# Performance work log

Measured on AMD Instinct MI355X. Metric: run time of the kernel, lower is better.

The kernel has to match this reference:

```python
import jax, jax.numpy as jnp
import numpy as np

N_NODES = 50000  # 4 node types x 12500
N_PER = 12500
E = 600000
H = 128
IN_DIMS = [128, 128, 64, 64]


def setup_inputs() -> dict:
    key = jax.random.key(0)
    ks = jax.random.split(key, 16)
    inp = {}
    for i, d in enumerate(IN_DIMS):
        inp[f"feat{i}"] = jax.random.normal(ks[i], (N_PER, d), dtype=jnp.float32)
        # xavier_normal-ish init, gain 1.414
        std = 1.414 * np.sqrt(2.0 / (d + H))
        inp[f"W_fc{i}"] = jax.random.normal(ks[4 + i], (d, H), dtype=jnp.float32) * std
        inp[f"b_fc{i}"] = jnp.zeros((H,), dtype=jnp.float32)
    inp["src"] = jax.random.randint(ks[8], (E,), 0, N_NODES, dtype=jnp.int32)
    inp["dst"] = jax.random.randint(ks[9], (E,), 0, N_NODES, dtype=jnp.int32)
    inp["e_feat"] = jax.random.randint(ks[10], (E,), 0, 36, dtype=jnp.int32)
    inp["b_g0"] = jnp.zeros((H,), dtype=jnp.float32)  # GraphConv layer0 (weight=False, bias)
    inp["W_g1"] = jax.random.normal(ks[11], (H, H), dtype=jnp.float32) * np.sqrt(1.0 / H)
    inp["b_g1"] = jnp.zeros((H,), dtype=jnp.float32)
    return inp


def _degree_norms(src, dst):
    ones = jnp.ones((src.shape[0],), dtype=jnp.float32)
    deg_out = jax.ops.segment_sum(ones, src, num_segments=N_NODES)
    deg_in = jax.ops.segment_sum(ones, dst, num_segments=N_NODES)
    # DGL norm='both': D_out^{-1/2} on src side, D_in^{-1/2} on dst side (clamp 0-degree)
    out_norm = jax.lax.rsqrt(jnp.maximum(deg_out, 1.0))
    in_norm = jax.lax.rsqrt(jnp.maximum(deg_in, 1.0))
    return out_norm, in_norm


def _gcn_aggregate(h, src, dst, out_norm, in_norm):
    m = (h * out_norm[:, None])[src]                      # [E, H] gather
    agg = jax.ops.segment_sum(m, dst, num_segments=N_NODES)
    return agg * in_norm[:, None]


def reference(feat0, feat1, feat2, feat3,
              W_fc0, b_fc0, W_fc1, b_fc1, W_fc2, b_fc2, W_fc3, b_fc3,
              src, dst, e_feat, b_g0, W_g1, b_g1):
    # per-node-type linear projections, then concat along node dim
    h = jnp.concatenate([
        feat0 @ W_fc0 + b_fc0,
        feat1 @ W_fc1 + b_fc1,
        feat2 @ W_fc2 + b_fc2,
        feat3 @ W_fc3 + b_fc3,
    ], axis=0)  # [N_NODES, H]

    out_norm, in_norm = _degree_norms(src, dst)
    # GraphConv layer 0: weight=False, bias, activation (dropout p=0 -> identity)
    h = jax.nn.relu(_gcn_aggregate(h, src, dst, out_norm, in_norm) + b_g0)
    # GraphConv layer 1: aggregate, then linear weight + bias, activation
    h = jax.nn.relu(_gcn_aggregate(h, src, dst, out_norm, in_norm) @ W_g1 + b_g1)

    e = e_feat.astype(jnp.float32)  # e_feat.reshape(-1,1).float() in original
    # forward graph: msg = ft + sum_{r in 0..4} where(e==r, ft, 0) = ft * (1 + 1{e in 0..4})
    w_fwd = 1.0 + sum((e == float(r)).astype(jnp.float32) for r in (0, 1, 2, 3, 4))
    agg_a = jax.ops.segment_sum(h[src] * w_fwd[:, None], dst, num_segments=N_NODES)
    # transpose graph (reversed edges, same e): msg = sum_{r in {6,14,30}} where(e==r, ft, 0)
    w_bwd = sum((e == float(r)).astype(jnp.float32) for r in (6, 14, 30))
    agg_b = jax.ops.segment_sum(h[dst] * w_bwd[:, None], src, num_segments=N_NODES)
    return agg_a + agg_b
```

## Files before the change

### kernel.cpp

```cpp
#include <hip/hip_runtime.h>
#include <hip/hip_bf16.h>

#define N_NODES 50000
#define N_PER   12500
#define E_EDGES 600000
#define HDIM    128

#define NBLK_BUILD ((E_EDGES + 255) / 256)
#define NBLK_FC    ((N_PER + 63) / 64)
#define BK_CAP  32
#define BKB_CAP 8
#define MASK31  0x7fffffff

#define HQ 32
#define HP 4
#define HSLICE (E_EDGES / HQ)

typedef __attribute__((ext_vector_type(8))) short bfrag;
typedef __attribute__((ext_vector_type(4))) float ffrag;

__device__ __forceinline__ unsigned short f2bf(float f) {
    union { float f; unsigned u; } x; x.f = f;
    unsigned r = x.u + 0x7fffu + ((x.u >> 16) & 1u);
    return (unsigned short)(r >> 16);
}
__device__ __forceinline__ float lo_bf(unsigned v) { return __uint_as_float(v << 16); }
__device__ __forceinline__ float hi_bf(unsigned v) { return __uint_as_float(v & 0xffff0000u); }
__device__ __forceinline__ unsigned pack2(float a, float b) {
    return (unsigned)f2bf(a) | ((unsigned)f2bf(b) << 16);
}
__device__ __forceinline__ float onrm_of(int deg) {
    return rsqrtf(fmaxf((float)deg, 1.0f));
}

__device__ __forceinline__ void acc8_add(float* acc, uint4 v) {
    acc[0] += lo_bf(v.x); acc[1] += hi_bf(v.x);
    acc[2] += lo_bf(v.y); acc[3] += hi_bf(v.y);
    acc[4] += lo_bf(v.z); acc[5] += hi_bf(v.z);
    acc[6] += lo_bf(v.w); acc[7] += hi_bf(v.w);
}
__device__ __forceinline__ void acc8_addw(float* acc, uint4 v, float w) {
    acc[0] += lo_bf(v.x) * w; acc[1] += hi_bf(v.x) * w;
    acc[2] += lo_bf(v.y) * w; acc[3] += hi_bf(v.y) * w;
    acc[4] += lo_bf(v.z) * w; acc[5] += hi_bf(v.z) * w;
    acc[6] += lo_bf(v.w) * w; acc[7] += hi_bf(v.w) * w;
}

__global__ __launch_bounds__(256) void prep_kernel(
    const float* __restrict__ W0, const float* __restrict__ W1,
    const float* __restrict__ W2, const float* __restrict__ W3,
    const float* __restrict__ Wg,
    const int* __restrict__ src,
    unsigned short* __restrict__ Wp, int* __restrict__ initp,
    unsigned short* __restrict__ partial) {
    __shared__ int hist[N_PER];
    int b = blockIdx.x;
    if (b < HQ * HP) {
        const int q = b >> 2;
        const int p = b & 3;
        for (int j = threadIdx.x; j < N_PER; j += 256) hist[j] = 0;
        __syncthreads();
        const int e0 = q * HSLICE;
        for (int i = e0 + threadIdx.x; i < e0 + HSLICE; i += 256) {
            int s = src[i];
            unsigned r = (unsigned)(s - p * N_PER);
            if (r < (unsigned)N_PER) atomicAdd(&hist[r], 1);
        }
        __syncthreads();
        unsigned short* out = partial + (size_t)q * N_NODES + (size_t)p * N_PER;
        for (int j = threadIdx.x; j < N_PER; j += 256)
            out[j] = (unsigned short)hist[j];
    } else if (b < HQ * HP + 32) {
        int tid = (b - HQ * HP) * 256 + threadIdx.x;
        const float* W; int D, base, off;
        if      (tid < 2048) { W = W0; D = 128; base = 0;    off = 0;     }
        else if (tid < 4096) { W = W1; D = 128; base = 2048; off = 16384; }
        else if (tid < 5120) { W = W2; D = 64;  base = 4096; off = 32768; }
        else if (tid < 6144) { W = W3; D = 64;  base = 5120; off = 40960; }
        else                 { W = Wg; D = 128; base = 6144; off = 49152; }
        int t2 = tid - base;
        int KT = D / 32;
        int l = t2 & 63;
        int tt = t2 >> 6;
        int kt = tt % KT, n0 = tt / KT;
        int n = n0 * 16 + (l & 15);
        int kb = kt * 32 + (l >> 4) * 8;
#pragma unroll
        for (int j = 0; j < 8; ++j)
            Wp[(size_t)off + (size_t)t2 * 8 + j] = f2bf(W[(size_t)(kb + j) * 128 + n]);
    } else {
        int blk = b - (HQ * HP + 32);
#pragma unroll
        for (int k = 0; k < 4; ++k) {
            int i = blk * 1024 + k * 256 + threadIdx.x;
            if (i < 4 * N_NODES)
                initp[i] = (i < 2 * N_NODES) ? -1 : 0;
        }
    }
}

template<int D>
__device__ __forceinline__ void fc_body(
    int blk, int tid,
    const float* __restrict__ X,
    const unsigned short* __restrict__ Wp,
    const float* __restrict__ bias,
    unsigned short* __restrict__ outbf,
    int rows)
{
    constexpr int KT = D / 32;
    const int lane = tid & 63;
    const int wave = tid >> 6;
    const int m = lane & 15, q = lane >> 4;
    const int rbase = blk * 64 + wave * 16;
    const int row = rbase + m;

    bfrag afr[KT];
#pragma unroll
    for (int kt = 0; kt < KT; ++kt) {
        bfrag a;
        if (row < rows) {
            const float* xp = X + (size_t)row * D + kt * 32 + q * 8;
            float4 u0 = *(const float4*)xp;
            float4 u1 = *(const float4*)(xp + 4);
            a[0] = (short)f2bf(u0.x); a[1] = (short)f2bf(u0.y);
            a[2] = (short)f2bf(u0.z); a[3] = (short)f2bf(u0.w);
            a[4] = (short)f2bf(u1.x); a[5] = (short)f2bf(u1.y);
            a[6] = (short)f2bf(u1.z); a[7] = (short)f2bf(u1.w);
        } else {
#pragma unroll
            for (int t = 0; t < 8; ++t) a[t] = 0;
        }
        afr[kt] = a;
    }

    ffrag acc[8];
#pragma unroll
    for (int n0 = 0; n0 < 8; ++n0)
#pragma unroll
        for (int t = 0; t < 4; ++t) acc[n0][t] = 0.f;

#pragma unroll
    for (int n0 = 0; n0 < 8; ++n0)
#pragma unroll
        for (int kt = 0; kt < KT; ++kt) {
            bfrag bfr = *(const bfrag*)(Wp + ((size_t)(n0 * KT + kt) * 64 + lane) * 8);
            acc[n0] = __builtin_amdgcn_mfma_f32_16x16x32_bf16(afr[kt], bfr, acc[n0], 0, 0, 0);
        }

#pragma unroll
    for (int n0 = 0; n0 < 8; ++n0) {
        const int col = n0 * 16 + m;
        const float bj = bias[col];
#pragma unroll
        for (int r = 0; r < 4; ++r) {
            int orow = rbase + q * 4 + r;
            if (orow < rows)
                outbf[(size_t)orow * 128 + col] = f2bf(acc[n0][r] + bj);
        }
    }
}

__global__ __launch_bounds__(256) void mega_kernel(
    const int* __restrict__ src, const int* __restrict__ dst,
    const int* __restrict__ ef,
    int* __restrict__ cnt_in, int* __restrict__ cntB,
    int* __restrict__ bucket, int* __restrict__ bucketB,
    int* __restrict__ head_ov, int* __restrict__ ov_pay, int* __restrict__ ov_nxt,
    int* __restrict__ head_ovB, int* __restrict__ ovB_pay, int* __restrict__ ovB_nxt,
    const float* __restrict__ f0, const float* __restrict__ f1,
    const float* __restrict__ f2, const float* __restrict__ f3,
    const unsigned short* __restrict__ Wp,
    const float* __restrict__ b0, const float* __restrict__ b1,
    const float* __restrict__ b2, const float* __restrict__ b3,
    unsigned short* __restrict__ Abf)
{
    const int b = blockIdx.x;
    if (b < NBLK_BUILD) {
        int e = b * 256 + threadIdx.x;
        if (e >= E_EDGES) return;
        int s = src[e], d = dst[e], t = ef[e];
        int v = s | ((t <= 4) ? 0x80000000 : 0);
        int p = atomicAdd(&cnt_in[d], 1);
        if (p < BK_CAP) bucket[d * BK_CAP + p] = v;
        else { ov_pay[e] = v; ov_nxt[e] = atomicExch(&head_ov[d], e); }
        if (t == 6 || t == 14 || t == 30) {
            int p2 = atomicAdd(&cntB[s], 1);
            if (p2 < BKB_CAP) bucketB[s * BKB_CAP + p2] = d;
            else { ovB_pay[e] = d; ovB_nxt[e] = atomicExch(&head_ovB[s], e); }
        }
    } else {
        int fb = b - NBLK_BUILD;
        int which = fb / NBLK_FC;
        int blk = fb - which * NBLK_FC;
        if (which == 0)
            fc_body<128>(blk, threadIdx.x, f0, Wp,         b0, Abf + (size_t)0 * N_PER * HDIM, N_PER);
        else if (which == 1)
            fc_body<128>(blk, threadIdx.x, f1, Wp + 16384, b1, Abf + (size_t)1 * N_PER * HDIM, N_PER);
        else if (which == 2)
            fc_body<64>(blk, threadIdx.x, f2, Wp + 32768, b2, Abf + (size_t)2 * N_PER * HDIM, N_PER);
        else
            fc_body<64>(blk, threadIdx.x, f3, Wp + 40960, b3, Abf + (size_t)3 * N_PER * HDIM, N_PER);
    }
}

__global__ __launch_bounds__(256) void scale_kernel(
    uint4* __restrict__ A, const unsigned short* __restrict__ partial,
    float* __restrict__ onrm_buf) {
    int idx = blockIdx.x * blockDim.x + threadIdx.x;
    int n = idx >> 4, j8 = idx & 15;
    int d = (int)partial[(size_t)j8 * N_NODES + n]
          + (int)partial[(size_t)(j8 + 16) * N_NODES + n];
    d += __shfl_xor(d, 1);
    d += __shfl_xor(d, 2);
    d += __shfl_xor(d, 4);
    d += __shfl_xor(d, 8);
    float on = onrm_of(d);
    if (j8 == 0) onrm_buf[n] = on;
    uint4 v = A[(size_t)n * 16 + j8];
    uint4 o;
    o.x = pack2(lo_bf(v.x) * on, hi_bf(v.x) * on);
    o.y = pack2(lo_bf(v.y) * on, hi_bf(v.y) * on);
    o.z = pack2(lo_bf(v.z) * on, hi_bf(v.z) * on);
    o.w = pack2(lo_bf(v.w) * on, hi_bf(v.w) * on);
    A[(size_t)n * 16 + j8] = o;
}

__global__ __launch_bounds__(256) void agg0_kernel(
    const uint4* __restrict__ A,
    const int* __restrict__ bucket, const int* __restrict__ cnt_in,
    const int* __restrict__ head_ov, const int* __restrict__ ov_pay,
    const int* __restrict__ ov_nxt,
    const float* __restrict__ onrm_buf, const float* __restrict__ b_g0,
    uint4* __restrict__ B) {
    int idx = blockIdx.x * blockDim.x + threadIdx.x;
    int n = idx >> 4, j8 = idx & 15;
    const int cnt = cnt_in[n];
    const int* bk = bucket + (size_t)n * BK_CAP;
    float acc[8] = {0.f, 0.f, 0.f, 0.f, 0.f, 0.f, 0.f, 0.f};
    int lim = min(cnt, BK_CAP);
    int i = 0;
    for (; i + 4 <= lim; i += 4) {
        int s0 = bk[i] & MASK31,     s1 = bk[i + 1] & MASK31;
        int s2 = bk[i + 2] & MASK31, s3 = bk[i + 3] & MASK31;
        uint4 v0 = A[(size_t)s0 * 16 + j8];
        uint4 v1 = A[(size_t)s1 * 16 + j8];
        uint4 v2 = A[(size_t)s2 * 16 + j8];
        uint4 v3 = A[(size_t)s3 * 16 + j8];
        acc8_add(acc, v0); acc8_add(acc, v1);
        acc8_add(acc, v2); acc8_add(acc, v3);
    }
    for (; i < lim; ++i) {
        int s = bk[i] & MASK31;
        acc8_add(acc, A[(size_t)s * 16 + j8]);
    }
    if (cnt > BK_CAP) {
        int e = head_ov[n];
        while (e >= 0) {
            int s = ov_pay[e] & MASK31;
            acc8_add(acc, A[(size_t)s * 16 + j8]);
            e = ov_nxt[e];
        }
    }
    float inr = onrm_of(cnt);
    float onr = onrm_buf[n];
    const float* bg = b_g0 + j8 * 8;
    float r[8];
#pragma unroll
    for (int k = 0; k < 8; ++k)
        r[k] = fmaxf(acc[k] * inr + bg[k], 0.f) * onr;
    uint4 o;
    o.x = pack2(r[0], r[1]); o.y = pack2(r[2], r[3]);
    o.z = pack2(r[4], r[5]); o.w = pack2(r[6], r[7]);
    B[(size_t)n * 16 + j8] = o;
}

__global__ __launch_bounds__(256) void gemm1_fused_kernel(
    const unsigned short* __restrict__ Bbf,
    const int* __restrict__ bucket, const int* __restrict__ cnt_in,
    const int* __restrict__ head_ov, const int* __restrict__ ov_pay,
    const int* __restrict__ ov_nxt,
    const unsigned short* __restrict__ Wp, const float* __restrict__ bias,
    unsigned short* __restrict__ outbf)
{
    const int lane = threadIdx.x & 63;
    const int wave = threadIdx.x >> 6;
    const int m = lane & 15, q = lane >> 4;
    const int rbase = blockIdx.x * 64 + wave * 16;
    const int node = rbase + m;

    float ga[32];
#pragma unroll
    for (int i = 0; i < 32; ++i) ga[i] = 0.f;

    if (node < N_NODES) {
        const int cnt = cnt_in[node];
        const int* bk = bucket + (size_t)node * BK_CAP;
        int lim = min(cnt, BK_CAP);
        int i = 0;
        for (; i + 2 <= lim; i += 2) {
            int s0 = bk[i] & MASK31, s1 = bk[i + 1] & MASK31;
            const uint4* r0 = (const uint4*)(Bbf + (size_t)s0 * 128);
            const uint4* r1 = (const uint4*)(Bbf + (size_t)s1 * 128);
            uint4 a0 = r0[0 * 4 + q], a1 = r0[1 * 4 + q], a2 = r0[2 * 4 + q], a3 = r0[3 * 4 + q];
            uint4 c0 = r1[0 * 4 + q], c1 = r1[1 * 4 + q], c2 = r1[2 * 4 + q], c3 = r1[3 * 4 + q];
            acc8_add(ga +  0, a0); acc8_add(ga +  8, a1);
            acc8_add(ga + 16, a2); acc8_add(ga + 24, a3);
            acc8_add(ga +  0, c0); acc8_add(ga +  8, c1);
            acc8_add(ga + 16, c2); acc8_add(ga + 24, c3);
        }
        for (; i < lim; ++i) {
            int s = bk[i] & MASK31;
            const uint4* rp = (const uint4*)(Bbf + (size_t)s * 128);
#pragma unroll
            for (int kt = 0; kt < 4; ++kt) acc8_add(ga + kt * 8, rp[kt * 4 + q]);
        }
        if (cnt > BK_CAP) {
            int e = head_ov[node];
            while (e >= 0) {
                int s = ov_pay[e] & MASK31;
                const uint4* rp = (const uint4*)(Bbf + (size_t)s * 128);
#pragma unroll
                for (int kt = 0; kt < 4; ++kt) acc8_add(ga + kt * 8, rp[kt * 4 + q]);
                e = ov_nxt[e];
            }
        }
    }

    bfrag afr[4];
#pragma unroll
    for (int kt = 0; kt < 4; ++kt)
#pragma unroll
        for (int j = 0; j < 8; ++j)
            afr[kt][j] = (short)f2bf(ga[kt * 8 + j]);

    ffrag acc[8];
#pragma unroll
    for (int n0 = 0; n0 < 8; ++n0)
#pragma unroll
        for (int t = 0; t < 4; ++t) acc[n0][t] = 0.f;

#pragma unroll
    for (int n0 = 0; n0 < 8; ++n0)
#pragma unroll
        for (int kt = 0; kt < 4; ++kt) {
            bfrag bfr = *(const bfrag*)(Wp + ((size_t)(n0 * 4 + kt) * 64 + lane) * 8);
            acc[n0] = __builtin_amdgcn_mfma_f32_16x16x32_bf16(afr[kt], bfr, acc[n0], 0, 0, 0);
        }

    float ir[4];
#pragma unroll
    for (int r = 0; r < 4; ++r) {
        int orow = rbase + q * 4 + r;
        ir[r] = (orow < N_NODES) ? onrm_of(cnt_in[orow]) : 0.f;
    }
#pragma unroll
    for (int n0 = 0; n0 < 8; ++n0) {
        const int col = n0 * 16 + m;
        const float bj = bias[col];
#pragma unroll
        for (int r = 0; r < 4; ++r) {
            int orow = rbase + q * 4 + r;
            if (orow < N_NODES)
                outbf[(size_t)orow * 128 + col] = f2bf(fmaxf(acc[n0][r] * ir[r] + bj, 0.f));
        }
    }
}

__global__ __launch_bounds__(256) void final_kernel(
    const uint4* __restrict__ H,
    const int* __restrict__ bucket, const int* __restrict__ cnt_in,
    const int* __restrict__ head_ov, const int* __restrict__ ov_pay,
    const int* __restrict__ ov_nxt,
    const int* __restrict__ bucketB, const int* __restrict__ cntB,
    const int* __restrict__ head_ovB, const int* __restrict__ ovB_pay,
    const int* __restrict__ ovB_nxt,
    float4* __restrict__ out4) {
    int idx = blockIdx.x * blockDim.x + threadIdx.x;
    int n = idx >> 4, j8 = idx & 15;
    float acc[8] = {0.f, 0.f, 0.f, 0.f, 0.f, 0.f, 0.f, 0.f};
    const int cnt = cnt_in[n];
    const int* bk = bucket + (size_t)n * BK_CAP;
    int lim = min(cnt, BK_CAP);
    int i = 0;
    for (; i + 4 <= lim; i += 4) {
        int c0 = bk[i], c1 = bk[i + 1], c2 = bk[i + 2], c3 = bk[i + 3];
        uint4 v0 = H[(size_t)(c0 & MASK31) * 16 + j8];
        uint4 v1 = H[(size_t)(c1 & MASK31) * 16 + j8];
        uint4 v2 = H[(size_t)(c2 & MASK31) * 16 + j8];
        uint4 v3 = H[(size_t)(c3 & MASK31) * 16 + j8];
        acc8_addw(acc, v0, (c0 < 0) ? 2.0f : 1.0f);
        acc8_addw(acc, v1, (c1 < 0) ? 2.0f : 1.0f);
        acc8_addw(acc, v2, (c2 < 0) ? 2.0f : 1.0f);
        acc8_addw(acc, v3, (c3 < 0) ? 2.0f : 1.0f);
    }
    for (; i < lim; ++i) {
        int c = bk[i];
        acc8_addw(acc, H[(size_t)(c & MASK31) * 16 + j8], (c < 0) ? 2.0f : 1.0f);
    }
    if (cnt > BK_CAP) {
        int e = head_ov[n];
        while (e >= 0) {
            int c = ov_pay[e];
            acc8_addw(acc, H[(size_t)(c & MASK31) * 16 + j8], (c < 0) ? 2.0f : 1.0f);
            e = ov_nxt[e];
        }
    }
    const int cb = cntB[n];
    const int* bkB = bucketB + (size_t)n * BKB_CAP;
    int limB = min(cb, BKB_CAP);
    for (int k = 0; k < limB; ++k) {
        int d = bkB[k];
        acc8_add(acc, H[(size_t)d * 16 + j8]);
    }
    if (cb > BKB_CAP) {
        int e = head_ovB[n];
        while (e >= 0) {
            acc8_add(acc, H[(size_t)ovB_pay[e] * 16 + j8]);
            e = ovB_nxt[e];
        }
    }
    float4 o0 = {acc[0], acc[1], acc[2], acc[3]};
    float4 o1 = {acc[4], acc[5], acc[6], acc[7]};
    out4[(size_t)n * 32 + j8 * 2]     = o0;
    out4[(size_t)n * 32 + j8 * 2 + 1] = o1;
}

extern "C" void kernel_launch(void* const* d_in, const int* in_sizes, int n_in,
                              void* d_out, int out_size, void* d_ws, size_t ws_size,
                              hipStream_t stream) {
    const float* feat[4]  = {(const float*)d_in[0], (const float*)d_in[3],
                             (const float*)d_in[6], (const float*)d_in[9]};
    const float* W_fc[4]  = {(const float*)d_in[1], (const float*)d_in[4],
                             (const float*)d_in[7], (const float*)d_in[10]};
    const float* b_fc[4]  = {(const float*)d_in[2], (const float*)d_in[5],
                             (const float*)d_in[8], (const float*)d_in[11]};
    const int*   src      = (const int*)d_in[12];
    const int*   dst      = (const int*)d_in[13];
    const int*   efeat    = (const int*)d_in[14];
    const float* b_g0     = (const float*)d_in[15];
    const float* W_g1     = (const float*)d_in[16];
    const float* b_g1     = (const float*)d_in[17];
    float* out = (float*)d_out;

    char* p = (char*)d_ws;
    unsigned short* Abf = (unsigned short*)p; p += (size_t)N_NODES * HDIM * 2;
    unsigned short* Bbf = (unsigned short*)p; p += (size_t)N_NODES * HDIM * 2;
    unsigned short* Wp  = (unsigned short*)p; p += (size_t)65536 * 2;
    int* bucket  = (int*)p; p += (size_t)N_NODES * BK_CAP * 4;
    int* bucketB = (int*)p; p += (size_t)N_NODES * BKB_CAP * 4;
    int* ov_pay  = (int*)p; p += (size_t)E_EDGES * 4;
    int* ov_nxt  = (int*)p; p += (size_t)E_EDGES * 4;
    int* ovB_pay = (int*)p; p += (size_t)E_EDGES * 4;
    int* ovB_nxt = (int*)p; p += (size_t)E_EDGES * 4;
    unsigned short* partial = (unsigned short*)p;
    p += (size_t)HQ * N_NODES * 2;
    float* onrm_buf = (float*)p; p += (size_t)N_NODES * 4;
    int* head_ov  = (int*)p; p += (size_t)N_NODES * 4;
    int* head_ovB = (int*)p; p += (size_t)N_NODES * 4;
    int* cnt_in   = (int*)p; p += (size_t)N_NODES * 4;
    int* cntB     = (int*)p; p += (size_t)N_NODES * 4;

    const unsigned short* Wpg = Wp + 49152;

    prep_kernel<<<HQ * HP + 32 + (4 * N_NODES + 1023) / 1024, 256, 0, stream>>>(
        W_fc[0], W_fc[1], W_fc[2], W_fc[3], W_g1, src, Wp, head_ov, partial);

    mega_kernel<<<NBLK_BUILD + 4 * NBLK_FC, 256, 0, stream>>>(
        src, dst, efeat, cnt_in, cntB,
        bucket, bucketB, head_ov, ov_pay, ov_nxt, head_ovB, ovB_pay, ovB_nxt,
        feat[0], feat[1], feat[2], feat[3], Wp,
        b_fc[0], b_fc[1], b_fc[2], b_fc[3], Abf);

    const int grid_node = (N_NODES * 16) / 256;

    scale_kernel<<<grid_node, 256, 0, stream>>>((uint4*)Abf, partial, onrm_buf);

    agg0_kernel<<<grid_node, 256, 0, stream>>>(
        (const uint4*)Abf, bucket, cnt_in, head_ov, ov_pay, ov_nxt,
        onrm_buf, b_g0, (uint4*)Bbf);

    gemm1_fused_kernel<<<(N_NODES + 63) / 64, 256, 0, stream>>>(
        Bbf, bucket, cnt_in, head_ov, ov_pay, ov_nxt, Wpg, b_g1, Abf);

    final_kernel<<<grid_node, 256, 0, stream>>>(
        (const uint4*)Abf, bucket, cnt_in, head_ov, ov_pay, ov_nxt,
        bucketB, cntB, head_ovB, ovB_pay, ovB_nxt, (float4*)out);
}
```

Baseline: 279.4 us.

## Replace capped buckets with overflow lists by deterministic CSR built via histograms and scan

Builds exact CSR adjacency for in-edges and selected reverse edges. It uses per-slice histograms, per-node plane prefix sums, a global scan, and a block-local shared-memory scatter, in place of fixed-capacity buckets with atomic linked-list overflow. Aggregation kernels then read contiguous neighbor ranges with no overflow chasing, and the workspace needs no init pass. In exchange it adds extra kernel launches, including a low-parallelism two-block scan, and reads the edge arrays several more times.

Result: slower. 412.4 us (+47.6%).

```diff
diff --git a/kernel.cpp b/kernel.cpp
--- a/kernel.cpp
+++ b/kernel.cpp
@@ -6,15 +6,13 @@
 #define E_EDGES 600000
 #define HDIM    128
 
-#define NBLK_BUILD ((E_EDGES + 255) / 256)
 #define NBLK_FC    ((N_PER + 63) / 64)
-#define BK_CAP  32
-#define BKB_CAP 8
 #define MASK31  0x7fffffff
 
 #define HQ 32
 #define HP 4
 #define HSLICE (E_EDGES / HQ)
+#define NBLK_SCAT (HQ * HP)
 
 typedef __attribute__((ext_vector_type(8))) short bfrag;
 typedef __attribute__((ext_vector_type(4))) float ffrag;
@@ -50,28 +48,50 @@
     const float* __restrict__ W0, const float* __restrict__ W1,
     const float* __restrict__ W2, const float* __restrict__ W3,
     const float* __restrict__ Wg,
-    const int* __restrict__ src,
-    unsigned short* __restrict__ Wp, int* __restrict__ initp,
-    unsigned short* __restrict__ partial) {
+    const int* __restrict__ src, const int* __restrict__ dst,
+    const int* __restrict__ ef,
+    unsigned short* __restrict__ Wp,
+    unsigned short* __restrict__ partialS,
+    unsigned short* __restrict__ partialD,
+    unsigned short* __restrict__ partialB) {
     __shared__ int hist[N_PER];
     int b = blockIdx.x;
-    if (b < HQ * HP) {
-        const int q = b >> 2;
-        const int p = b & 3;
+    if (b < 3 * NBLK_SCAT) {
+        const int which = b / NBLK_SCAT;
+        const int r = b - which * NBLK_SCAT;
+        const int q = r >> 2;
+        const int p = r & 3;
+        const int g0 = p * N_PER;
         for (int j = threadIdx.x; j < N_PER; j += 256) hist[j] = 0;
         __syncthreads();
         const int e0 = q * HSLICE;
-        for (int i = e0 + threadIdx.x; i < e0 + HSLICE; i += 256) {
-            int s = src[i];
-            unsigned r = (unsigned)(s - p * N_PER);
-            if (r < (unsigned)N_PER) atomicAdd(&hist[r], 1);
+        if (which == 0) {
+            for (int i = e0 + threadIdx.x; i < e0 + HSLICE; i += 256) {
+                unsigned rr = (unsigned)(src[i] - g0);
+                if (rr < (unsigned)N_PER) atomicAdd(&hist[rr], 1);
+            }
+        } else if (which == 1) {
+            for (int i = e0 + threadIdx.x; i < e0 + HSLICE; i += 256) {
+                unsigned rr = (unsigned)(dst[i] - g0);
+                if (rr < (unsigned)N_PER) atomicAdd(&hist[rr], 1);
+            }
+        } else {
+            for (int i = e0 + threadIdx.x; i < e0 + HSLICE; i += 256) {
+                int t = ef[i];
+                if (t == 6 || t == 14 || t == 30) {
+                    unsigned rr = (unsigned)(src[i] - g0);
+                    if (rr < (unsigned)N_PER) atomicAdd(&hist[rr], 1);
+                }
+            }
         }
         __syncthreads();
-        unsigned short* out = partial + (size_t)q * N_NODES + (size_t)p * N_PER;
+        unsigned short* out =
+            (which == 0 ? partialS : which == 1 ? partialD : partialB)
+            + (size_t)q * N_NODES + g0;
         for (int j = threadIdx.x; j < N_PER; j += 256)
             out[j] = (unsigned short)hist[j];
-    } else if (b < HQ * HP + 32) {
-        int tid = (b - HQ * HP) * 256 + threadIdx.x;
+    } else {
+        int tid = (b - 3 * NBLK_SCAT) * 256 + threadIdx.x;
         const float* W; int D, base, off;
         if      (tid < 2048) { W = W0; D = 128; base = 0;    off = 0;     }
         else if (tid < 4096) { W = W1; D = 128; base = 2048; off = 16384; }
@@ -88,14 +108,59 @@
 #pragma unroll
         for (int j = 0; j < 8; ++j)
             Wp[(size_t)off + (size_t)t2 * 8 + j] = f2bf(W[(size_t)(kb + j) * 128 + n]);
-    } else {
-        int blk = b - (HQ * HP + 32);
-#pragma unroll
-        for (int k = 0; k < 4; ++k) {
-            int i = blk * 1024 + k * 256 + threadIdx.x;
-            if (i < 4 * N_NODES)
-                initp[i] = (i < 2 * N_NODES) ? -1 : 0;
-        }
+    }
+}
+
+__global__ __launch_bounds__(256) void plane_prefix_kernel(
+    unsigned short* __restrict__ partialD, unsigned short* __restrict__ partialB,
+    int* __restrict__ degD, int* __restrict__ degB) {
+    int n = blockIdx.x * 256 + threadIdx.x;
+    if (n >= N_NODES) return;
+    int run = 0;
+#pragma unroll
+    for (int q = 0; q < HQ; ++q) {
+        size_t ix = (size_t)q * N_NODES + n;
+        int c = partialD[ix];
+        partialD[ix] = (unsigned short)run;
+        run += c;
+    }
+    degD[n] = run;
+    run = 0;
+#pragma unroll
+    for (int q = 0; q < HQ; ++q) {
+        size_t ix = (size_t)q * N_NODES + n;
+        int c = partialB[ix];
+        partialB[ix] = (unsigned short)run;
+        run += c;
+    }
+    degB[n] = run;
+}
+
+__global__ __launch_bounds__(1024) void scan_kernel(
+    const int* __restrict__ degD, int* __restrict__ scanD,
+    const int* __restrict__ degB, int* __restrict__ scanB) {
+    const int* deg = blockIdx.x ? degB : degD;
+    int* sc = blockIdx.x ? scanB : scanD;
+    __shared__ int part[1024];
+    const int t = threadIdx.x;
+    const int n0 = t * 49;
+    int s = 0;
+    for (int i = 0; i < 49; ++i) {
+        int n = n0 + i;
+        s += (n < N_NODES) ? deg[n] : 0;
+    }
+    part[t] = s;
+    __syncthreads();
+    for (int off = 1; off < 1024; off <<= 1) {
+        int x = (t >= off) ? part[t - off] : 0;
+        __syncthreads();
+        part[t] += x;
+        __syncthreads();
+    }
+    int run = (t == 0) ? 0 : part[t - 1];
+    for (int i = 0; i < 49; ++i) {
+        int n = n0 + i;
+        if (n < N_NODES) { sc[n] = run; run += deg[n]; }
     }
 }
 
@@ -164,10 +229,10 @@
 __global__ __launch_bounds__(256) void mega_kernel(
     const int* __restrict__ src, const int* __restrict__ dst,
     const int* __restrict__ ef,
-    int* __restrict__ cnt_in, int* __restrict__ cntB,
+    const unsigned short* __restrict__ prefD,
+    const unsigned short* __restrict__ prefB,
+    const int* __restrict__ scanD, const int* __restrict__ scanB,
     int* __restrict__ bucket, int* __restrict__ bucketB,
-    int* __restrict__ head_ov, int* __restrict__ ov_pay, int* __restrict__ ov_nxt,
-    int* __restrict__ head_ovB, int* __restrict__ ovB_pay, int* __restrict__ ovB_nxt,
     const float* __restrict__ f0, const float* __restrict__ f1,
     const float* __restrict__ f2, const float* __restrict__ f3,
     const unsigned short* __restrict__ Wp,
@@ -175,22 +240,41 @@
     const float* __restrict__ b2, const float* __restrict__ b3,
     unsigned short* __restrict__ Abf)
 {
+    __shared__ int offD[N_PER];
+    __shared__ int offB[N_PER / 2];
     const int b = blockIdx.x;
-    if (b < NBLK_BUILD) {
-        int e = b * 256 + threadIdx.x;
-        if (e >= E_EDGES) return;
-        int s = src[e], d = dst[e], t = ef[e];
-        int v = s | ((t <= 4) ? 0x80000000 : 0);
-        int p = atomicAdd(&cnt_in[d], 1);
-        if (p < BK_CAP) bucket[d * BK_CAP + p] = v;
-        else { ov_pay[e] = v; ov_nxt[e] = atomicExch(&head_ov[d], e); }
-        if (t == 6 || t == 14 || t == 30) {
-            int p2 = atomicAdd(&cntB[s], 1);
-            if (p2 < BKB_CAP) bucketB[s * BKB_CAP + p2] = d;
-            else { ovB_pay[e] = d; ovB_nxt[e] = atomicExch(&head_ovB[s], e); }
+    if (b < NBLK_SCAT) {
+        const int q = b >> 2;
+        const int p = b & 3;
+        const int g0 = p * N_PER;
+        for (int j = threadIdx.x; j < N_PER; j += 256)
+            offD[j] = scanD[g0 + j] + (int)prefD[(size_t)q * N_NODES + g0 + j];
+        for (int w = threadIdx.x; w < N_PER / 2; w += 256) {
+            int lo = scanB[g0 + 2 * w]     + (int)prefB[(size_t)q * N_NODES + g0 + 2 * w];
+            int hi = scanB[g0 + 2 * w + 1] + (int)prefB[(size_t)q * N_NODES + g0 + 2 * w + 1];
+            offB[w] = lo | (hi << 16);
+        }
+        __syncthreads();
+        const int e0 = q * HSLICE;
+        for (int i = e0 + threadIdx.x; i < e0 + HSLICE; i += 256) {
+            int s = src[i], d = dst[i], t = ef[i];
+            unsigned rd = (unsigned)(d - g0);
+            if (rd < (unsigned)N_PER) {
+                int slot = atomicAdd(&offD[rd], 1);
+                bucket[slot] = s | ((t <= 4) ? 0x80000000 : 0);
+            }
+            if (t == 6 || t == 14 || t == 30) {
+                unsigned rs = (unsigned)(s - g0);
+                if (rs < (unsigned)N_PER) {
+                    unsigned inc = (rs & 1) ? 0x10000u : 1u;
+                    unsigned old = atomicAdd((unsigned*)&offB[rs >> 1], inc);
+                    int slot = (rs & 1) ? (int)(old >> 16) : (int)(old & 0xFFFFu);
+                    bucketB[slot] = d;
+                }
+            }
         }
     } else {
-        int fb = b - NBLK_BUILD;
+        int fb = b - NBLK_SCAT;
         int which = fb / NBLK_FC;
         int blk = fb - which * NBLK_FC;
         if (which == 0)
@@ -205,12 +289,12 @@
 }
 
 __global__ __launch_bounds__(256) void scale_kernel(
-    uint4* __restrict__ A, const unsigned short* __restrict__ partial,
+    uint4* __restrict__ A, const unsigned short* __restrict__ partialS,
     float* __restrict__ onrm_buf) {
     int idx = blockIdx.x * blockDim.x + threadIdx.x;
     int n = idx >> 4, j8 = idx & 15;
-    int d = (int)partial[(size_t)j8 * N_NODES + n]
-          + (int)partial[(size_t)(j8 + 16) * N_NODES + n];
+    int d = (int)partialS[(size_t)j8 * N_NODES + n]
+          + (int)partialS[(size_t)(j8 + 16) * N_NODES + n];
     d += __shfl_xor(d, 1);
     d += __shfl_xor(d, 2);
     d += __shfl_xor(d, 4);
@@ -228,19 +312,17 @@
 
 __global__ __launch_bounds__(256) void agg0_kernel(
     const uint4* __restrict__ A,
-    const int* __restrict__ bucket, const int* __restrict__ cnt_in,
-    const int* __restrict__ head_ov, const int* __restrict__ ov_pay,
-    const int* __restrict__ ov_nxt,
+    const int* __restrict__ bucket, const int* __restrict__ scanD,
+    const int* __restrict__ degD,
     const float* __restrict__ onrm_buf, const float* __restrict__ b_g0,
     uint4* __restrict__ B) {
     int idx = blockIdx.x * blockDim.x + threadIdx.x;
     int n = idx >> 4, j8 = idx & 15;
-    const int cnt = cnt_in[n];
-    const int* bk = bucket + (size_t)n * BK_CAP;
+    const int cnt = degD[n];
+    const int* bk = bucket + scanD[n];
     float acc[8] = {0.f, 0.f, 0.f, 0.f, 0.f, 0.f, 0.f, 0.f};
-    int lim = min(cnt, BK_CAP);
     int i = 0;
-    for (; i + 4 <= lim; i += 4) {
+    for (; i + 4 <= cnt; i += 4) {
         int s0 = bk[i] & MASK31,     s1 = bk[i + 1] & MASK31;
         int s2 = bk[i + 2] & MASK31, s3 = bk[i + 3] & MASK31;
         uint4 v0 = A[(size_t)s0 * 16 + j8];
@@ -250,17 +332,9 @@
         acc8_add(acc, v0); acc8_add(acc, v1);
         acc8_add(acc, v2); acc8_add(acc, v3);
     }
-    for (; i < lim; ++i) {
+    for (; i < cnt; ++i) {
         int s = bk[i] & MASK31;
         acc8_add(acc, A[(size_t)s * 16 + j8]);
-    }
-    if (cnt > BK_CAP) {
-        int e = head_ov[n];
-        while (e >= 0) {
-            int s = ov_pay[e] & MASK31;
-            acc8_add(acc, A[(size_t)s * 16 + j8]);
-            e = ov_nxt[e];
-        }
     }
     float inr = onrm_of(cnt);
     float onr = onrm_buf[n];
@@ -277,9 +351,8 @@
 
 __global__ __launch_bounds__(256) void gemm1_fused_kernel(
     const unsigned short* __restrict__ Bbf,
-    const int* __restrict__ bucket, const int* __restrict__ cnt_in,
-    const int* __restrict__ head_ov, const int* __restrict__ ov_pay,
-    const int* __restrict__ ov_nxt,
+    const int* __restrict__ bucket, const int* __restrict__ scanD,
+    const int* __restrict__ degD,
     const unsigned short* __restrict__ Wp, const float* __restrict__ bias,
     unsigned short* __restrict__ outbf)
 {
@@ -294,11 +367,10 @@
     for (int i = 0; i < 32; ++i) ga[i] = 0.f;
 
     if (node < N_NODES) {
-        const int cnt = cnt_in[node];
-        const int* bk = bucket + (size_t)node * BK_CAP;
-        int lim = min(cnt, BK_CAP);
+        const int cnt = degD[node];
+        const int* bk = bucket + scanD[node];
         int i = 0;
-        for (; i + 2 <= lim; i += 2) {
+        for (; i + 2 <= cnt; i += 2) {
             int s0 = bk[i] & MASK31, s1 = bk[i + 1] & MASK31;
             const uint4* r0 = (const uint4*)(Bbf + (size_t)s0 * 128);
             const uint4* r1 = (const uint4*)(Bbf + (size_t)s1 * 128);
@@ -309,21 +381,11 @@
             acc8_add(ga +  0, c0); acc8_add(ga +  8, c1);
             acc8_add(ga + 16, c2); acc8_add(ga + 24, c3);
         }
-        for (; i < lim; ++i) {
+        for (; i < cnt; ++i) {
             int s = bk[i] & MASK31;
             const uint4* rp = (const uint4*)(Bbf + (size_t)s * 128);
 #pragma unroll
             for (int kt = 0; kt < 4; ++kt) acc8_add(ga + kt * 8, rp[kt * 4 + q]);
-        }
-        if (cnt > BK_CAP) {
-            int e = head_ov[node];
-            while (e >= 0) {
-                int s = ov_pay[e] & MASK31;
-                const uint4* rp = (const uint4*)(Bbf + (size_t)s * 128);
-#pragma unroll
-                for (int kt = 0; kt < 4; ++kt) acc8_add(ga + kt * 8, rp[kt * 4 + q]);
-                e = ov_nxt[e];
-            }
         }
     }
 
@@ -352,7 +414,7 @@
 #pragma unroll
     for (int r = 0; r < 4; ++r) {
         int orow = rbase + q * 4 + r;
-        ir[r] = (orow < N_NODES) ? onrm_of(cnt_in[orow]) : 0.f;
+        ir[r] = (orow < N_NODES) ? onrm_of(degD[orow]) : 0.f;
     }
 #pragma unroll
     for (int n0 = 0; n0 < 8; ++n0) {
@@ -369,21 +431,18 @@
 
 __global__ __launch_bounds__(256) void final_kernel(
     const uint4* __restrict__ H,
-    const int* __restrict__ bucket, const int* __restrict__ cnt_in,
-    const int* __restrict__ head_ov, const int* __restrict__ ov_pay,
-    const int* __restrict__ ov_nxt,
-    const int* __restrict__ bucketB, const int* __restrict__ cntB,
-    const int* __restrict__ head_ovB, const int* __restrict__ ovB_pay,
-    const int* __restrict__ ovB_nxt,
+    const int* __restrict__ bucket, const int* __restrict__ scanD,
+    const int* __restrict__ degD,
+    const int* __restrict__ bucketB, const int* __restrict__ scanB,
+    const int* __restrict__ degB,
     float4* __restrict__ out4) {
     int idx = blockIdx.x * blockDim.x + threadIdx.x;
     int n = idx >> 4, j8 = idx & 15;
     float acc[8] = {0.f, 0.f, 0.f, 0.f, 0.f, 0.f, 0.f, 0.f};
-    const int cnt = cnt_in[n];
-    const int* bk = bucket + (size_t)n * BK_CAP;
-    int lim = min(cnt, BK_CAP);
+    const int cnt = degD[n];
+    const int* bk = bucket + scanD[n];
     int i = 0;
-    for (; i + 4 <= lim; i += 4) {
+    for (; i + 4 <= cnt; i += 4) {
         int c0 = bk[i], c1 = bk[i + 1], c2 = bk[i + 2], c3 = bk[i + 3];
         uint4 v0 = H[(size_t)(c0 & MASK31) * 16 + j8];
         uint4 v1 = H[(size_t)(c1 & MASK31) * 16 + j8];
@@ -394,31 +453,15 @@
         acc8_addw(acc, v2, (c2 < 0) ? 2.0f : 1.0f);
         acc8_addw(acc, v3, (c3 < 0) ? 2.0f : 1.0f);
     }
-    for (; i < lim; ++i) {
+    for (; i < cnt; ++i) {
         int c = bk[i];
         acc8_addw(acc, H[(size_t)(c & MASK31) * 16 + j8], (c < 0) ? 2.0f : 1.0f);
     }
-    if (cnt > BK_CAP) {
-        int e = head_ov[n];
-        while (e >= 0) {
-            int c = ov_pay[e];
-            acc8_addw(acc, H[(size_t)(c & MASK31) * 16 + j8], (c < 0) ? 2.0f : 1.0f);
-            e = ov_nxt[e];
-        }
-    }
-    const int cb = cntB[n];
-    const int* bkB = bucketB + (size_t)n * BKB_CAP;
-    int limB = min(cb, BKB_CAP);
-    for (int k = 0; k < limB; ++k) {
+    const int cb = degB[n];
+    const int* bkB = bucketB + scanB[n];
+    for (int k = 0; k < cb; ++k) {
         int d = bkB[k];
         acc8_add(acc, H[(size_t)d * 16 + j8]);
-    }
-    if (cb > BKB_CAP) {
-        int e = head_ovB[n];
-        while (e >= 0) {
-            acc8_add(acc, H[(size_t)ovB_pay[e] * 16 + j8]);
-            e = ovB_nxt[e];
-        }
     }
     float4 o0 = {acc[0], acc[1], acc[2], acc[3]};
     float4 o1 = {acc[4], acc[5], acc[6], acc[7]};
@@ -447,43 +490,43 @@
     unsigned short* Abf = (unsigned short*)p; p += (size_t)N_NODES * HDIM * 2;
     unsigned short* Bbf = (unsigned short*)p; p += (size_t)N_NODES * HDIM * 2;
     unsigned short* Wp  = (unsigned short*)p; p += (size_t)65536 * 2;
-    int* bucket  = (int*)p; p += (size_t)N_NODES * BK_CAP * 4;
-    int* bucketB = (int*)p; p += (size_t)N_NODES * BKB_CAP * 4;
-    int* ov_pay  = (int*)p; p += (size_t)E_EDGES * 4;
-    int* ov_nxt  = (int*)p; p += (size_t)E_EDGES * 4;
-    int* ovB_pay = (int*)p; p += (size_t)E_EDGES * 4;
-    int* ovB_nxt = (int*)p; p += (size_t)E_EDGES * 4;
-    unsigned short* partial = (unsigned short*)p;
-    p += (size_t)HQ * N_NODES * 2;
+    int* bucket  = (int*)p; p += (size_t)E_EDGES * 4;
+    int* bucketB = (int*)p; p += (size_t)E_EDGES * 4;
+    unsigned short* partialS = (unsigned short*)p; p += (size_t)HQ * N_NODES * 2;
+    unsigned short* partialD = (unsigned short*)p; p += (size_t)HQ * N_NODES * 2;
+    unsigned short* partialB = (unsigned short*)p; p += (size_t)HQ * N_NODES * 2;
+    int* degD  = (int*)p; p += (size_t)N_NODES * 4;
+    int* degB  = (int*)p; p += (size_t)N_NODES * 4;
+    int* scanD = (int*)p; p += (size_t)N_NODES * 4;
+    int* scanB = (int*)p; p += (size_t)N_NODES * 4;
     float* onrm_buf = (float*)p; p += (size_t)N_NODES * 4;
-    int* head_ov  = (int*)p; p += (size_t)N_NODES * 4;
-    int* head_ovB = (int*)p; p += (size_t)N_NODES * 4;
-    int* cnt_in   = (int*)p; p += (size_t)N_NODES * 4;
-    int* cntB     = (int*)p; p += (size_t)N_NODES * 4;
 
     const unsigned short* Wpg = Wp + 49152;
 
-    prep_kernel<<<HQ * HP + 32 + (4 * N_NODES + 1023) / 1024, 256, 0, stream>>>(
-        W_fc[0], W_fc[1], W_fc[2], W_fc[3], W_g1, src, Wp, head_ov, partial);
-
-    mega_kernel<<<NBLK_BUILD + 4 * NBLK_FC, 256, 0, stream>>>(
-        src, dst, efeat, cnt_in, cntB,
-        bucket, bucketB, head_ov, ov_pay, ov_nxt, head_ovB, ovB_pay, ovB_nxt,
+    prep_kernel<<<3 * NBLK_SCAT + 32, 256, 0, stream>>>(
+        W_fc[0], W_fc[1], W_fc[2], W_fc[3], W_g1, src, dst, efeat,
+        Wp, partialS, partialD, partialB);
+
+    plane_prefix_kernel<<<(N_NODES + 255) / 256, 256, 0, stream>>>(
+        partialD, partialB, degD, degB);
+
+    scan_kernel<<<2, 1024, 0, stream>>>(degD, scanD, degB, scanB);
+
+    mega_kernel<<<NBLK_SCAT + 4 * NBLK_FC, 256, 0, stream>>>(
+        src, dst, efeat, partialD, partialB, scanD, scanB, bucket, bucketB,
         feat[0], feat[1], feat[2], feat[3], Wp,
         b_fc[0], b_fc[1], b_fc[2], b_fc[3], Abf);
 
     const int grid_node = (N_NODES * 16) / 256;
 
-    scale_kernel<<<grid_node, 256, 0, stream>>>((uint4*)Abf, partial, onrm_buf);
+    scale_kernel<<<grid_node, 256, 0, stream>>>((uint4*)Abf, partialS, onrm_buf);
 
     agg0_kernel<<<grid_node, 256, 0, stream>>>(
-        (const uint4*)Abf, bucket, cnt_in, head_ov, ov_pay, ov_nxt,
-        onrm_buf, b_g0, (uint4*)Bbf);
+        (const uint4*)Abf, bucket, scanD, degD, onrm_buf, b_g0, (uint4*)Bbf);
 
     gemm1_fused_kernel<<<(N_NODES + 63) / 64, 256, 0, stream>>>(
-        Bbf, bucket, cnt_in, head_ov, ov_pay, ov_nxt, Wpg, b_g1, Abf);
+        Bbf, bucket, scanD, degD, Wpg, b_g1, Abf);
 
     final_kernel<<<grid_node, 256, 0, stream>>>(
-        (const uint4*)Abf, bucket, cnt_in, head_ov, ov_pay, ov_nxt,
-        bucketB, cntB, head_ovB, ovB_pay, ovB_nxt, (float4*)out);
-}
+        (const uint4*)Abf, bucket, scanD, degD, bucketB, scanB, degB, (float4*)out);
+}
```
